# Kernel tuning notes

Measured on AMD Instinct MI355X. Metric: run time of the kernel, lower is better.

## Reference

```python
import jax, jax.numpy as jnp
import numpy as np

N, E, D, A, FC, B = 50000, 800000, 256, 7, 64, 512
EPS = 1e-5

def _glorot(key, fan_in, fan_out):
    lim = np.sqrt(6.0 / (fan_in + fan_out))
    return jax.random.uniform(key, (fan_in, fan_out), jnp.float32, -lim, lim)

def setup_inputs() -> dict:
    key = jax.random.key(0)
    ks = jax.random.split(key, 20)
    inp = {
        'x': jax.random.normal(ks[0], (N, 3), jnp.float32),
        'edge_index': jax.random.randint(ks[1], (2, E), 0, N, jnp.int32),
        'batch_index': jnp.sort(jax.random.randint(ks[2], (N,), 0, B, jnp.int32)),
        'a': jax.random.normal(ks[3], (B, A), jnp.float32),
        # GCNConv weights (lin weight + bias)
        'W0': _glorot(ks[4], 3, D),   'b0': jnp.zeros((D,), jnp.float32),
        'W1': _glorot(ks[5], D, D),   'b1': jnp.zeros((D,), jnp.float32),
        'W2': _glorot(ks[6], D, D),   'b2': jnp.zeros((D,), jnp.float32),
        'W3': _glorot(ks[7], D, D),   'b3': jnp.zeros((D,), jnp.float32),
        # action MLP
        'afc1_w': _glorot(ks[8], A, 8 * A),     'afc1_b': jnp.zeros((8 * A,), jnp.float32),
        'afc2_w': _glorot(ks[9], 8 * A, 8 * A), 'afc2_b': jnp.zeros((8 * A,), jnp.float32),
        'afc3_w': _glorot(ks[10], 8 * A, D),    'afc3_b': jnp.zeros((D,), jnp.float32),
        # head
        'fc1_w': _glorot(ks[11], D, FC), 'fc1_b': jnp.zeros((FC,), jnp.float32),
        'fc2_w': _glorot(ks[12], FC, 1), 'fc2_b': jnp.zeros((1,), jnp.float32),
        # LayerNorm affine params
        'ln1_g': jnp.ones((D,), jnp.float32),  'ln1_b': jnp.zeros((D,), jnp.float32),
        'ln2_g': jnp.ones((D,), jnp.float32),  'ln2_b': jnp.zeros((D,), jnp.float32),
        'ln4_g': jnp.ones((FC,), jnp.float32), 'ln4_b': jnp.zeros((FC,), jnp.float32),
        'ln5_g': jnp.ones((8 * A,), jnp.float32), 'ln5_b': jnp.zeros((8 * A,), jnp.float32),
    }
    return inp

def leaky(x):
    return jnp.where(x >= 0, x, 0.01 * x)

def layernorm(x, g, b):
    m = jnp.mean(x, axis=-1, keepdims=True)
    v = jnp.mean((x - m) ** 2, axis=-1, keepdims=True)
    return (x - m) * jax.lax.rsqrt(v + EPS) * g + b

def reference(x, edge_index, batch_index, a,
              W0, b0, W1, b1, W2, b2, W3, b3,
              afc1_w, afc1_b, afc2_w, afc2_b, afc3_w, afc3_b,
              fc1_w, fc1_b, fc2_w, fc2_b,
              ln1_g, ln1_b, ln2_g, ln2_b, ln4_g, ln4_b, ln5_g, ln5_b):
    n = x.shape[0]
    loop = jnp.arange(n, dtype=edge_index.dtype)
    src = jnp.concatenate([edge_index[0], loop])  # message sources
    dst = jnp.concatenate([edge_index[1], loop])  # message targets
    # symmetric GCN normalization with self-loops: deg over targets
    deg = jax.ops.segment_sum(jnp.ones_like(dst, dtype=x.dtype), dst, num_segments=n)
    dinv = jnp.where(deg > 0, jax.lax.rsqrt(deg), 0.0)
    norm = (dinv[src] * dinv[dst])[:, None]  # [E+N, 1]

    def gcn(h, W, bias):
        hw = h @ W
        agg = jax.ops.segment_sum(hw[src] * norm, dst, num_segments=n)
        return agg + bias

    h0 = gcn(x, W0, b0)
    h1 = leaky(gcn(h0, W1, b1)) + h0
    h2 = leaky(gcn(h1, W2, b2)) + h1
    h3 = leaky(gcn(h2, W3, b3)) + h2

    pooled = jax.ops.segment_max(h3, batch_index, num_segments=B)  # [B, D]
    V = layernorm(pooled, ln2_g, ln2_b)

    av = leaky(a @ afc1_w + afc1_b)
    av = layernorm(av, ln5_g, ln5_b)
    av = leaky(av @ afc2_w + afc2_b)
    av = leaky(av @ afc3_w + afc3_b)
    av = layernorm(av, ln1_g, ln1_b)

    z = V * av
    z = layernorm(leaky(z @ fc1_w + fc1_b), ln4_g, ln4_b)
    out = z @ fc2_w + fc2_b
    return out[:, 0]
```

## Files before the change

kernel.cpp:

```cpp
#include <hip/hip_runtime.h>

#define LN_EPS 1e-5f
#define SCAN_CHUNK 4096

typedef __bf16 bf16x8 __attribute__((ext_vector_type(8)));
typedef float f32x4 __attribute__((ext_vector_type(4)));
typedef float f32x2 __attribute__((ext_vector_type(2)));

__device__ __forceinline__ float b2f(unsigned short s) {
    union { unsigned u; float f; } c; c.u = ((unsigned)s) << 16; return c.f;
}
__device__ __forceinline__ unsigned short f2b(float f) {
    union { float f; unsigned u; } c; c.f = f;
    unsigned r = (c.u + 0x7FFFu + ((c.u >> 16) & 1u)) >> 16;
    return (unsigned short)r;
}
__device__ __forceinline__ f32x2 up2(unsigned u) {
    union { unsigned u; float f; } lo, hi;
    lo.u = u << 16; hi.u = u & 0xffff0000u;
    f32x2 r; r.x = lo.f; r.y = hi.f; return r;
}
__device__ __forceinline__ unsigned pk2(f32x2 v) {
    return ((unsigned)f2b(v.y) << 16) | (unsigned)f2b(v.x);
}
__device__ __forceinline__ float leaky(float x) { return x >= 0.f ? x : 0.01f * x; }
__device__ __forceinline__ unsigned encf(float f) {
    union { float f; unsigned u; } c; c.f = f;
    return ((int)c.u < 0) ? ~c.u : (c.u | 0x80000000u);
}
__device__ __forceinline__ float decf(unsigned u) {
    union { unsigned u; float f; } c;
    c.u = (u & 0x80000000u) ? (u & 0x7FFFFFFFu) : ~u;
    return c.f;
}


__global__ void init_kernel(int* ec, int* fill, int n) {
    int i = blockIdx.x * 256 + threadIdx.x;
    if (i < n) { ec[i] = 0; fill[i] = 0; }
}

__global__ void deg_kernel(const int* __restrict__ dst, int* ec, int e) {
    int i = blockIdx.x * 256 + threadIdx.x;
    if (i < e) atomicAdd(&ec[dst[i]], 1);
}

__global__ void scanA(const int* __restrict__ ec, int* __restrict__ bsum, int n) {
    __shared__ int red[4];
    int b = blockIdx.x, t = threadIdx.x;
    int base = b * SCAN_CHUNK + t * 16;
    int s = 0;
    #pragma unroll
    for (int k = 0; k < 16; ++k) { int i = base + k; if (i < n) s += (ec[i] + 7) & ~7; }
    #pragma unroll
    for (int off = 32; off; off >>= 1) s += __shfl_down(s, off, 64);
    if ((t & 63) == 0) red[t >> 6] = s;
    __syncthreads();
    if (t == 0) bsum[b] = red[0] + red[1] + red[2] + red[3];
}

__global__ void scanB(int* bsum, int nb) {
    if (threadIdx.x == 0) {
        int acc = 0;
        for (int i = 0; i < nb; ++i) { int v = bsum[i]; bsum[i] = acc; acc += v; }
        bsum[nb] = acc;
    }
}

__global__ void scanC(const int* __restrict__ ec, const int* __restrict__ bsum,
                      int* __restrict__ ptr, int n, int nb) {
    __shared__ int wsum[4];
    int b = blockIdx.x, t = threadIdx.x, lane = t & 63, w = t >> 6;
    int base = b * SCAN_CHUNK + t * 16;
    int loc[16]; int s = 0;
    #pragma unroll
    for (int k = 0; k < 16; ++k) {
        int i = base + k; int v = (i < n) ? ((ec[i] + 7) & ~7) : 0;
        loc[k] = s; s += v;
    }
    int x = s;
    #pragma unroll
    for (int off = 1; off < 64; off <<= 1) { int y = __shfl_up(x, off, 64); if (lane >= off) x += y; }
    if (lane == 63) wsum[w] = x;
    __syncthreads();
    int wexcl = 0;
    #pragma unroll
    for (int ww = 0; ww < 4; ++ww) if (ww < w) wexcl += wsum[ww];
    int toff = bsum[b] + wexcl + (x - s);
    #pragma unroll
    for (int k = 0; k < 16; ++k) { int i = base + k; if (i < n) ptr[i] = toff + loc[k]; }
    if (b == nb - 1 && t == 255) ptr[n] = bsum[nb];
}

__global__ void dinv_kernel(const int* __restrict__ ec, float* __restrict__ dinv, int n, int mpad) {
    int i = blockIdx.x * 256 + threadIdx.x;
    if (i < mpad) dinv[i] = (i < n) ? rsqrtf((float)(ec[i] + 1)) : 0.f;
}

__global__ void xp_kernel(const float* __restrict__ x, const float* __restrict__ dinv,
                          float4* __restrict__ xp, int n, int mpad) {
    int i = blockIdx.x * 256 + threadIdx.x;
    if (i >= mpad) return;
    float4 v = make_float4(0.f, 0.f, 0.f, 0.f);
    if (i < n) {
        float d = dinv[i];
        v.x = d * x[i * 3]; v.y = d * x[i * 3 + 1]; v.z = d * x[i * 3 + 2];
    }
    xp[i] = v;
}

__global__ void csrc_init_kernel(const int* __restrict__ ptr, int* __restrict__ csrc, int n) {
    int i = blockIdx.x * 256 + threadIdx.x;
    if (i < ptr[n]) csrc[i] = n << 6;
}

__global__ void fill_kernel(const int* __restrict__ src, const int* __restrict__ dst,
                            const int* __restrict__ ptr, int* fill,
                            int* __restrict__ csrc, int e) {
    int i = blockIdx.x * 256 + threadIdx.x;
    if (i < e) {
        int d = dst[i];
        int pos = atomicAdd(&fill[d], 1);
        csrc[ptr[d] + pos] = src[i] << 6;
    }
}


__global__ void wt_kernel(const float* __restrict__ W1, const float* __restrict__ W2,
                          const float* __restrict__ W3, unsigned short* __restrict__ wt) {
    int k = blockIdx.x, l = blockIdx.y, nn = threadIdx.x;
    const float* W = (l == 0) ? W1 : (l == 1) ? W2 : W3;
    wt[l * 65536 + nn * 256 + k] = f2b(W[k * 256 + nn]);
}


__global__ void aggx_kernel(const float4* __restrict__ xp, const float* __restrict__ dinv,
                            const int* __restrict__ ptr, const int* __restrict__ csrc,
                            float* __restrict__ aggx, int n) {
    int i = blockIdx.x * 256 + threadIdx.x;
    if (i >= n) return;
    const char* xb = (const char*)xp;
    float4 self = xp[i];
    float a0 = self.x, a1 = self.y, a2 = self.z;
    float p0 = 0.f, p1 = 0.f, p2 = 0.f;
    float q0 = 0.f, q1 = 0.f, q2 = 0.f;
    float r0 = 0.f, r1 = 0.f, r2 = 0.f;
    int e0 = ptr[i], e1 = ptr[i + 1];
    for (int e = e0; e < e1; e += 4) {
        int4 v = *(const int4*)(csrc + e);
        float4 u0 = *(const float4*)(xb + (((unsigned)v.x) >> 2));
        float4 u1 = *(const float4*)(xb + (((unsigned)v.y) >> 2));
        float4 u2 = *(const float4*)(xb + (((unsigned)v.z) >> 2));
        float4 u3 = *(const float4*)(xb + (((unsigned)v.w) >> 2));
        a0 += u0.x; a1 += u0.y; a2 += u0.z;
        p0 += u1.x; p1 += u1.y; p2 += u1.z;
        q0 += u2.x; q1 += u2.y; q2 += u2.z;
        r0 += u3.x; r1 += u3.y; r2 += u3.z;
    }
    a0 += (p0 + q0) + r0; a1 += (p1 + q1) + r1; a2 += (p2 + q2) + r2;
    float di = dinv[i];
    aggx[i * 3] = a0 * di; aggx[i * 3 + 1] = a1 * di; aggx[i * 3 + 2] = a2 * di;
}

__global__ __launch_bounds__(256) void h0_kernel(const float* __restrict__ aggx,
                          const float* __restrict__ W0, const float* __restrict__ b0,
                          const float* __restrict__ dinv,
                          float* __restrict__ h, unsigned short* __restrict__ hbs,
                          int n, int mpad) {
    int t = threadIdx.x;
    int row = blockIdx.x * 4 + (t >> 6);
    int f = (t & 63) * 4;
    if (row >= mpad) return;
    unsigned short* hp = hbs + ((size_t)(f >> 5) * mpad + row) * 32 + (f & 31);
    if (row < n) {
        float a0 = aggx[row * 3], a1 = aggx[row * 3 + 1], a2 = aggx[row * 3 + 2];
        float4 w0 = *(const float4*)(W0 + f);
        float4 w1 = *(const float4*)(W0 + 256 + f);
        float4 w2 = *(const float4*)(W0 + 512 + f);
        float4 bb = *(const float4*)(b0 + f);
        float4 v;
        v.x = bb.x + a0 * w0.x + a1 * w1.x + a2 * w2.x;
        v.y = bb.y + a0 * w0.y + a1 * w1.y + a2 * w2.y;
        v.z = bb.z + a0 * w0.z + a1 * w1.z + a2 * w2.z;
        v.w = bb.w + a0 * w0.w + a1 * w1.w + a2 * w2.w;
        *(float4*)(h + (size_t)row * 256 + f) = v;
        float di = dinv[row];
        ushort4 o;
        o.x = f2b(di * v.x); o.y = f2b(di * v.y); o.z = f2b(di * v.z); o.w = f2b(di * v.w);
        *(ushort4*)hp = o;
    } else {
        ushort4 o; o.x = 0; o.y = 0; o.z = 0; o.w = 0;
        *(ushort4*)hp = o;
    }
}


__global__ __launch_bounds__(256) void spmm_kernel(
    const unsigned short* __restrict__ hbs,
    const int* __restrict__ ptr, const int* __restrict__ csrc,
    const float* __restrict__ dinv,
    unsigned short* __restrict__ agg,
    int n, int mpad) {
    int chunk = blockIdx.x & 7;
    int g = blockIdx.x >> 3;
    int t = threadIdx.x;
    int node = g * 64 + (t >> 2);
    if (node >= n) return;
    unsigned loff = (unsigned)((t & 3) << 4);
    const char* cb = (const char*)hbs + (size_t)chunk * mpad * 64;
    int e0 = ptr[node], e1 = ptr[node + 1];
    uint4 own = *(const uint4*)(cb + (((unsigned)node << 6) | loff));
    f32x2 accA0 = up2(own.x), accA1 = up2(own.y), accA2 = up2(own.z), accA3 = up2(own.w);
    f32x2 accB0 = (f32x2)(0.f), accB1 = (f32x2)(0.f), accB2 = (f32x2)(0.f), accB3 = (f32x2)(0.f);
    int e = e0;
    int4 ia, ib;
    if (e < e1) { ia = *(const int4*)(csrc + e); ib = *(const int4*)(csrc + e + 4); }
    while (e < e1) {
        int en = e + 8;
        int4 na, nb;
        if (en < e1) { na = *(const int4*)(csrc + en); nb = *(const int4*)(csrc + en + 4); }
        uint4 u0 = *(const uint4*)(cb + ((unsigned)ia.x | loff));
        uint4 u1 = *(const uint4*)(cb + ((unsigned)ia.y | loff));
        uint4 u2 = *(const uint4*)(cb + ((unsigned)ia.z | loff));
        uint4 u3 = *(const uint4*)(cb + ((unsigned)ia.w | loff));
        uint4 u4 = *(const uint4*)(cb + ((unsigned)ib.x | loff));
        uint4 u5 = *(const uint4*)(cb + ((unsigned)ib.y | loff));
        uint4 u6 = *(const uint4*)(cb + ((unsigned)ib.z | loff));
        uint4 u7 = *(const uint4*)(cb + ((unsigned)ib.w | loff));
        accA0 += up2(u0.x); accA1 += up2(u0.y); accA2 += up2(u0.z); accA3 += up2(u0.w);
        accB0 += up2(u1.x); accB1 += up2(u1.y); accB2 += up2(u1.z); accB3 += up2(u1.w);
        accA0 += up2(u2.x); accA1 += up2(u2.y); accA2 += up2(u2.z); accA3 += up2(u2.w);
        accB0 += up2(u3.x); accB1 += up2(u3.y); accB2 += up2(u3.z); accB3 += up2(u3.w);
        accA0 += up2(u4.x); accA1 += up2(u4.y); accA2 += up2(u4.z); accA3 += up2(u4.w);
        accB0 += up2(u5.x); accB1 += up2(u5.y); accB2 += up2(u5.z); accB3 += up2(u5.w);
        accA0 += up2(u6.x); accA1 += up2(u6.y); accA2 += up2(u6.z); accA3 += up2(u6.w);
        accB0 += up2(u7.x); accB1 += up2(u7.y); accB2 += up2(u7.z); accB3 += up2(u7.w);
        ia = na; ib = nb; e = en;
    }
    float di = dinv[node];
    f32x2 dd; dd.x = di; dd.y = di;
    accA0 = (accA0 + accB0) * dd;
    accA1 = (accA1 + accB1) * dd;
    accA2 = (accA2 + accB2) * dd;
    accA3 = (accA3 + accB3) * dd;
    uint4 o;
    o.x = pk2(accA0); o.y = pk2(accA1); o.z = pk2(accA2); o.w = pk2(accA3);
    *(uint4*)((char*)agg + (size_t)chunk * mpad * 64 + (((unsigned)node << 6) | loff)) = o;
}


__global__ __launch_bounds__(256) void gemm_kernel(const unsigned short* __restrict__ A,
                                                   const unsigned short* __restrict__ Bt,
                                                   const float* __restrict__ bias,
                                                   const float* __restrict__ dinv,
                                                   float* __restrict__ h,
                                                   unsigned short* __restrict__ hbs,
                                                   const int* __restrict__ batch,
                                                   unsigned* __restrict__ pooledu,
                                                   int mpad, int n, int write_hbs, int last) {
    const int K = 256;
    __shared__ int sb[64];
    int wid = threadIdx.x >> 6, lane = threadIdx.x & 63;
    int m0 = blockIdx.x * 64;
    if (last && threadIdx.x < 64) {
        int r = m0 + threadIdx.x;
        sb[threadIdx.x] = (r < n) ? batch[r] : -1;
    }
    __syncthreads();
    int n0 = wid * 64;
    int lr = lane & 15, lg = lane >> 4;
    f32x4 acc[4][4];
    #pragma unroll
    for (int i = 0; i < 4; i++)
        #pragma unroll
        for (int j = 0; j < 4; j++) acc[i][j] = (f32x4)(0.f);
    const unsigned short* Ap = A + ((size_t)(m0 + lr)) * 32 + lg * 8;
    const unsigned short* Bp = Bt + (size_t)(n0 + lr) * K + lg * 8;
    #pragma unroll
    for (int kc = 0; kc < 8; ++kc) {
        bf16x8 af[4], bfr[4];
        #pragma unroll
        for (int mi = 0; mi < 4; mi++)
            af[mi] = *(const bf16x8*)(Ap + (size_t)kc * mpad * 32 + mi * 512);
        #pragma unroll
        for (int ni = 0; ni < 4; ni++)
            bfr[ni] = *(const bf16x8*)(Bp + (size_t)ni * 16 * K + kc * 32);
        #pragma unroll
        for (int mi = 0; mi < 4; mi++)
            #pragma unroll
            for (int ni = 0; ni < 4; ni++)
                acc[mi][ni] = __builtin_amdgcn_mfma_f32_16x16x32_bf16(af[mi], bfr[ni], acc[mi][ni], 0, 0, 0);
    }
    if (!last) {
        #pragma unroll
        for (int mi = 0; mi < 4; mi++) {
            int r0 = m0 + mi * 16 + lg * 4;
            float4 dv = *(const float4*)(dinv + r0);
            #pragma unroll
            for (int ni = 0; ni < 4; ni++) {
                int c = n0 + ni * 16 + lr;
                float bv = bias[c];
                int ch = c >> 5, cf = c & 31;
                float vr[4];
                #pragma unroll
                for (int j = 0; j < 4; ++j) {
                    size_t ho = (size_t)(r0 + j) * 256 + c;
                    float v = leaky(acc[mi][ni][j] + bv) + h[ho];
                    h[ho] = v;
                    vr[j] = v;
                }
                if (write_hbs) {
                    unsigned short* hp = hbs + ((size_t)ch * mpad + r0) * 32 + cf;
                    hp[0]  = f2b(vr[0] * dv.x);
                    hp[32] = f2b(vr[1] * dv.y);
                    hp[64] = f2b(vr[2] * dv.z);
                    hp[96] = f2b(vr[3] * dv.w);
                }
            }
        }
    } else {
        #pragma unroll
        for (int ni = 0; ni < 4; ni++) {
            int c = n0 + ni * 16 + lr;
            float bv = bias[c];
            int cs = -1; float cm = 0.f;
            #pragma unroll
            for (int mi = 0; mi < 4; mi++) {
                int rb = mi * 16 + lg * 4;
                #pragma unroll
                for (int j = 0; j < 4; ++j) {
                    int seg = sb[rb + j];
                    float v = leaky(acc[mi][ni][j] + bv) + h[(size_t)(m0 + rb + j) * 256 + c];
                    if (seg >= 0) {
                        if (seg != cs) {
                            if (cs >= 0) atomicMax(pooledu + (size_t)cs * 256 + c, encf(cm));
                            cs = seg; cm = v;
                        } else {
                            cm = fmaxf(cm, v);
                        }
                    }
                }
            }
            if (cs >= 0) atomicMax(pooledu + (size_t)cs * 256 + c, encf(cm));
        }
    }
}

__global__ void pool_init_kernel(unsigned* pooledu) {
    pooledu[blockIdx.x * 256 + threadIdx.x] = 0u;
}


__device__ __forceinline__ float blk_sum(float v, float* red) {
    #pragma unroll
    for (int off = 32; off; off >>= 1) v += __shfl_down(v, off, 64);
    int lane = threadIdx.x & 63, wid = threadIdx.x >> 6;
    if (lane == 0) red[wid] = v;
    __syncthreads();
    float s = red[0] + red[1] + red[2] + red[3];
    __syncthreads();
    return s;
}

__global__ __launch_bounds__(256) void head_kernel(
    const unsigned* __restrict__ pooledu, const float* __restrict__ a,
    const float* __restrict__ afc1_w, const float* __restrict__ afc1_b,
    const float* __restrict__ afc2_w, const float* __restrict__ afc2_b,
    const float* __restrict__ afc3_w, const float* __restrict__ afc3_b,
    const float* __restrict__ fc1_w, const float* __restrict__ fc1_b,
    const float* __restrict__ fc2_w, const float* __restrict__ fc2_b,
    const float* __restrict__ ln1_g, const float* __restrict__ ln1_b,
    const float* __restrict__ ln2_g, const float* __restrict__ ln2_b,
    const float* __restrict__ ln4_g, const float* __restrict__ ln4_b,
    const float* __restrict__ ln5_g, const float* __restrict__ ln5_b,
    float* __restrict__ out) {
    __shared__ float red[4];
    __shared__ float sM[2];
    __shared__ float s1[56], s2[56], sZ[256], sT[64];
    int b = blockIdx.x, tid = threadIdx.x;

    float pv = decf(pooledu[(size_t)b * 256 + tid]);
    float m = blk_sum(pv, red) * (1.f / 256.f);
    float d0 = pv - m;
    float var = blk_sum(d0 * d0, red) * (1.f / 256.f);
    float V = d0 * rsqrtf(var + LN_EPS) * ln2_g[tid] + ln2_b[tid];

    if (tid < 56) {
        float acc = afc1_b[tid];
        #pragma unroll
        for (int k = 0; k < 7; ++k) acc += a[b * 7 + k] * afc1_w[k * 56 + tid];
        s1[tid] = leaky(acc);
    }
    __syncthreads();
    if (tid == 0) {
        float s = 0.f; for (int k = 0; k < 56; ++k) s += s1[k];
        float mm = s / 56.f;
        float q = 0.f; for (int k = 0; k < 56; ++k) { float d = s1[k] - mm; q += d * d; }
        sM[0] = mm; sM[1] = rsqrtf(q / 56.f + LN_EPS);
    }
    __syncthreads();
    if (tid < 56) s1[tid] = (s1[tid] - sM[0]) * sM[1] * ln5_g[tid] + ln5_b[tid];
    __syncthreads();
    if (tid < 56) {
        float acc = afc2_b[tid];
        for (int k = 0; k < 56; ++k) acc += s1[k] * afc2_w[k * 56 + tid];
        s2[tid] = leaky(acc);
    }
    __syncthreads();
    float acc = afc3_b[tid];
    for (int k = 0; k < 56; ++k) acc += s2[k] * afc3_w[k * 256 + tid];
    acc = leaky(acc);
    m = blk_sum(acc, red) * (1.f / 256.f);
    d0 = acc - m;
    var = blk_sum(d0 * d0, red) * (1.f / 256.f);
    float av = d0 * rsqrtf(var + LN_EPS) * ln1_g[tid] + ln1_b[tid];

    float z = V * av;
    sZ[tid] = z;
    __syncthreads();
    if (tid < 64) {
        float a2 = fc1_b[tid];
        for (int k = 0; k < 256; ++k) a2 += sZ[k] * fc1_w[k * 64 + tid];
        sT[tid] = leaky(a2);
    }
    __syncthreads();
    if (tid == 0) {
        float s = 0.f; for (int k = 0; k < 64; ++k) s += sT[k];
        float mm = s / 64.f;
        float q = 0.f; for (int k = 0; k < 64; ++k) { float d = sT[k] - mm; q += d * d; }
        float r = rsqrtf(q / 64.f + LN_EPS);
        float o = fc2_b[0];
        for (int k = 0; k < 64; ++k) {
            float zz = (sT[k] - mm) * r * ln4_g[k] + ln4_b[k];
            o += zz * fc2_w[k];
        }
        out[b] = o;
    }
}


extern "C" void kernel_launch(void* const* d_in, const int* in_sizes, int n_in,
                              void* d_out, int out_size, void* d_ws, size_t ws_size,
                              hipStream_t stream) {
    const float* x     = (const float*)d_in[0];
    const int*   eidx  = (const int*)d_in[1];
    const int*   batch = (const int*)d_in[2];
    const float* a     = (const float*)d_in[3];
    const float* W0 = (const float*)d_in[4];  const float* b0 = (const float*)d_in[5];
    const float* W1 = (const float*)d_in[6];  const float* b1 = (const float*)d_in[7];
    const float* W2 = (const float*)d_in[8];  const float* b2 = (const float*)d_in[9];
    const float* W3 = (const float*)d_in[10]; const float* b3 = (const float*)d_in[11];
    const float* afc1_w = (const float*)d_in[12]; const float* afc1_b = (const float*)d_in[13];
    const float* afc2_w = (const float*)d_in[14]; const float* afc2_b = (const float*)d_in[15];
    const float* afc3_w = (const float*)d_in[16]; const float* afc3_b = (const float*)d_in[17];
    const float* fc1_w  = (const float*)d_in[18]; const float* fc1_b  = (const float*)d_in[19];
    const float* fc2_w  = (const float*)d_in[20]; const float* fc2_b  = (const float*)d_in[21];
    const float* ln1_g = (const float*)d_in[22]; const float* ln1_b = (const float*)d_in[23];
    const float* ln2_g = (const float*)d_in[24]; const float* ln2_b = (const float*)d_in[25];
    const float* ln4_g = (const float*)d_in[26]; const float* ln4_b = (const float*)d_in[27];
    const float* ln5_g = (const float*)d_in[28]; const float* ln5_b = (const float*)d_in[29];

    int N = in_sizes[0] / 3;
    int E = in_sizes[1] / 2;
    int B = in_sizes[3] / 7;
    int Mpad = ((N + 63) / 64) * 64;
    int NB = (N + SCAN_CHUNK - 1) / SCAN_CHUNK;
    int Ecap = E + 7 * N + 8;

    char* p = (char*)d_ws;
    auto alloc = [&](size_t bytes) -> char* {
        char* r = p; p += (bytes + 255) & ~(size_t)255; return r;
    };
    int*   ec   = (int*)alloc((size_t)N * 4);
    int*   fill = (int*)alloc((size_t)N * 4);
    int*   ptr  = (int*)alloc((size_t)(N + 1) * 4);
    int*   bsum = (int*)alloc((size_t)(NB + 1) * 4);
    int*   csrc = (int*)alloc((size_t)Ecap * 4);
    float* dinv = (float*)alloc((size_t)Mpad * 4);
    float4* xp  = (float4*)alloc((size_t)Mpad * 16);
    float* aggx = (float*)alloc((size_t)N * 3 * 4);
    float* h    = (float*)alloc((size_t)Mpad * 256 * 4);
    unsigned short* hbs = (unsigned short*)alloc((size_t)Mpad * 256 * 2);
    unsigned short* agg = (unsigned short*)alloc((size_t)Mpad * 256 * 2);
    unsigned short* wt  = (unsigned short*)alloc((size_t)3 * 65536 * 2);
    unsigned* pooledu = (unsigned*)alloc((size_t)B * 256 * 4);

    const int* srcl = eidx;
    const int* dstl = eidx + E;

    init_kernel<<<(N + 255) / 256, 256, 0, stream>>>(ec, fill, N);
    deg_kernel<<<(E + 255) / 256, 256, 0, stream>>>(dstl, ec, E);
    scanA<<<NB, 256, 0, stream>>>(ec, bsum, N);
    scanB<<<1, 64, 0, stream>>>(bsum, NB);
    scanC<<<NB, 256, 0, stream>>>(ec, bsum, ptr, N, NB);
    dinv_kernel<<<(Mpad + 255) / 256, 256, 0, stream>>>(ec, dinv, N, Mpad);
    xp_kernel<<<(Mpad + 255) / 256, 256, 0, stream>>>(x, dinv, xp, N, Mpad);
    csrc_init_kernel<<<(Ecap + 255) / 256, 256, 0, stream>>>(ptr, csrc, N);
    fill_kernel<<<(E + 255) / 256, 256, 0, stream>>>(srcl, dstl, ptr, fill, csrc, E);
    wt_kernel<<<dim3(256, 3), 256, 0, stream>>>(W1, W2, W3, wt);
    aggx_kernel<<<(N + 255) / 256, 256, 0, stream>>>(xp, dinv, ptr, csrc, aggx, N);
    h0_kernel<<<Mpad / 4, 256, 0, stream>>>(aggx, W0, b0, dinv, h, hbs, N, Mpad);
    pool_init_kernel<<<B, 256, 0, stream>>>(pooledu);

    const float* biases[3] = { b1, b2, b3 };
    int nblkN = (N + 63) / 64;
    for (int l = 0; l < 3; ++l) {
        spmm_kernel<<<nblkN * 8, 256, 0, stream>>>(hbs, ptr, csrc, dinv, agg, N, Mpad);
        gemm_kernel<<<Mpad / 64, 256, 0, stream>>>(agg, wt + (size_t)l * 65536, biases[l],
                                                   dinv, h, hbs, batch, pooledu,
                                                   Mpad, N, (l < 2) ? 1 : 0, (l == 2) ? 1 : 0);
    }

    head_kernel<<<B, 256, 0, stream>>>(pooledu, a,
        afc1_w, afc1_b, afc2_w, afc2_b, afc3_w, afc3_b,
        fc1_w, fc1_b, fc2_w, fc2_b,
        ln1_g, ln1_b, ln2_g, ln2_b, ln4_g, ln4_b, ln5_g, ln5_b,
        (float*)d_out);
}
```

Measured before the change: 561.3 us.

## Drop fp32 residual buffer; rebuild residual from scaled bf16 features and merge setup kernels

Removes the fp32 hidden-state array h (Mpad×256 floats) that was read and written in every GEMM epilogue. The residual is now recovered from the bf16 dinv-scaled copy hbs by multiplying by sqrt(degree), using a new sdeg array. The epilogue updates hbs in place. It also merges dinv, xp and csrc padding initialisation into one node_setup kernel, which pads only the per-node tail slots. In exchange, the residual path now runs in bf16, adding rounding error that accumulates across layers.

After: 506.1 us. -9.8%, faster.

```diff
diff --git a/kernel.cpp b/kernel.cpp
--- a/kernel.cpp
+++ b/kernel.cpp
@@ -92,26 +92,25 @@
     if (b == nb - 1 && t == 255) ptr[n] = bsum[nb];
 }
 
-__global__ void dinv_kernel(const int* __restrict__ ec, float* __restrict__ dinv, int n, int mpad) {
-    int i = blockIdx.x * 256 + threadIdx.x;
-    if (i < mpad) dinv[i] = (i < n) ? rsqrtf((float)(ec[i] + 1)) : 0.f;
-}
-
-__global__ void xp_kernel(const float* __restrict__ x, const float* __restrict__ dinv,
-                          float4* __restrict__ xp, int n, int mpad) {
+__global__ void node_setup(const float* __restrict__ x, const int* __restrict__ ec,
+                           const int* __restrict__ ptr,
+                           float* __restrict__ dinv, float* __restrict__ sdeg,
+                           float4* __restrict__ xp, int* __restrict__ csrc,
+                           int n, int mpad) {
     int i = blockIdx.x * 256 + threadIdx.x;
     if (i >= mpad) return;
+    float dv = 0.f, sv = 0.f;
     float4 v = make_float4(0.f, 0.f, 0.f, 0.f);
     if (i < n) {
-        float d = dinv[i];
-        v.x = d * x[i * 3]; v.y = d * x[i * 3 + 1]; v.z = d * x[i * 3 + 2];
-    }
-    xp[i] = v;
-}
-
-__global__ void csrc_init_kernel(const int* __restrict__ ptr, int* __restrict__ csrc, int n) {
-    int i = blockIdx.x * 256 + threadIdx.x;
-    if (i < ptr[n]) csrc[i] = n << 6;
+        int e = ec[i];
+        float dg = (float)(e + 1);
+        dv = rsqrtf(dg); sv = sqrtf(dg);
+        v.x = dv * x[i * 3]; v.y = dv * x[i * 3 + 1]; v.z = dv * x[i * 3 + 2];
+        int p0 = ptr[i] + e, p1 = ptr[i] + ((e + 7) & ~7);
+        int pad = n << 6;
+        for (int j = p0; j < p1; ++j) csrc[j] = pad;
+    }
+    dinv[i] = dv; sdeg[i] = sv; xp[i] = v;
 }
 
 __global__ void fill_kernel(const int* __restrict__ src, const int* __restrict__ dst,
@@ -165,7 +164,7 @@
 __global__ __launch_bounds__(256) void h0_kernel(const float* __restrict__ aggx,
                           const float* __restrict__ W0, const float* __restrict__ b0,
                           const float* __restrict__ dinv,
-                          float* __restrict__ h, unsigned short* __restrict__ hbs,
+                          unsigned short* __restrict__ hbs,
                           int n, int mpad) {
     int t = threadIdx.x;
     int row = blockIdx.x * 4 + (t >> 6);
@@ -183,7 +182,6 @@
         v.y = bb.y + a0 * w0.y + a1 * w1.y + a2 * w2.y;
         v.z = bb.z + a0 * w0.z + a1 * w1.z + a2 * w2.z;
         v.w = bb.w + a0 * w0.w + a1 * w1.w + a2 * w2.w;
-        *(float4*)(h + (size_t)row * 256 + f) = v;
         float di = dinv[row];
         ushort4 o;
         o.x = f2b(di * v.x); o.y = f2b(di * v.y); o.z = f2b(di * v.z); o.w = f2b(di * v.w);
@@ -253,11 +251,11 @@
                                                    const unsigned short* __restrict__ Bt,
                                                    const float* __restrict__ bias,
                                                    const float* __restrict__ dinv,
-                                                   float* __restrict__ h,
+                                                   const float* __restrict__ sdeg,
                                                    unsigned short* __restrict__ hbs,
                                                    const int* __restrict__ batch,
                                                    unsigned* __restrict__ pooledu,
-                                                   int mpad, int n, int write_hbs, int last) {
+                                                   int mpad, int n, int last) {
     const int K = 256;
     __shared__ int sb[64];
     int wid = threadIdx.x >> 6, lane = threadIdx.x & 63;
@@ -296,26 +294,25 @@
         for (int mi = 0; mi < 4; mi++) {
             int r0 = m0 + mi * 16 + lg * 4;
             float4 dv = *(const float4*)(dinv + r0);
+            float4 sv = *(const float4*)(sdeg + r0);
             #pragma unroll
             for (int ni = 0; ni < 4; ni++) {
                 int c = n0 + ni * 16 + lr;
                 float bv = bias[c];
                 int ch = c >> 5, cf = c & 31;
-                float vr[4];
-                #pragma unroll
-                for (int j = 0; j < 4; ++j) {
-                    size_t ho = (size_t)(r0 + j) * 256 + c;
-                    float v = leaky(acc[mi][ni][j] + bv) + h[ho];
-                    h[ho] = v;
-                    vr[j] = v;
-                }
-                if (write_hbs) {
-                    unsigned short* hp = hbs + ((size_t)ch * mpad + r0) * 32 + cf;
-                    hp[0]  = f2b(vr[0] * dv.x);
-                    hp[32] = f2b(vr[1] * dv.y);
-                    hp[64] = f2b(vr[2] * dv.z);
-                    hp[96] = f2b(vr[3] * dv.w);
-                }
+                unsigned short* hp = hbs + ((size_t)ch * mpad + r0) * 32 + cf;
+                float h0o = b2f(hp[0])  * sv.x;
+                float h1o = b2f(hp[32]) * sv.y;
+                float h2o = b2f(hp[64]) * sv.z;
+                float h3o = b2f(hp[96]) * sv.w;
+                float v0 = leaky(acc[mi][ni][0] + bv) + h0o;
+                float v1 = leaky(acc[mi][ni][1] + bv) + h1o;
+                float v2 = leaky(acc[mi][ni][2] + bv) + h2o;
+                float v3 = leaky(acc[mi][ni][3] + bv) + h3o;
+                hp[0]  = f2b(v0 * dv.x);
+                hp[32] = f2b(v1 * dv.y);
+                hp[64] = f2b(v2 * dv.z);
+                hp[96] = f2b(v3 * dv.w);
             }
         }
     } else {
@@ -323,14 +320,18 @@
         for (int ni = 0; ni < 4; ni++) {
             int c = n0 + ni * 16 + lr;
             float bv = bias[c];
+            int ch = c >> 5, cf = c & 31;
+            const unsigned short* hpb = hbs + (size_t)ch * mpad * 32 + cf;
             int cs = -1; float cm = 0.f;
             #pragma unroll
             for (int mi = 0; mi < 4; mi++) {
                 int rb = mi * 16 + lg * 4;
                 #pragma unroll
                 for (int j = 0; j < 4; ++j) {
+                    int row = m0 + rb + j;
                     int seg = sb[rb + j];
-                    float v = leaky(acc[mi][ni][j] + bv) + h[(size_t)(m0 + rb + j) * 256 + c];
+                    float ho = b2f(hpb[(size_t)row * 32]) * sdeg[row];
+                    float v = leaky(acc[mi][ni][j] + bv) + ho;
                     if (seg >= 0) {
                         if (seg != cs) {
                             if (cs >= 0) atomicMax(pooledu + (size_t)cs * 256 + c, encf(cm));
@@ -477,9 +478,9 @@
     int*   bsum = (int*)alloc((size_t)(NB + 1) * 4);
     int*   csrc = (int*)alloc((size_t)Ecap * 4);
     float* dinv = (float*)alloc((size_t)Mpad * 4);
+    float* sdeg = (float*)alloc((size_t)Mpad * 4);
     float4* xp  = (float4*)alloc((size_t)Mpad * 16);
     float* aggx = (float*)alloc((size_t)N * 3 * 4);
-    float* h    = (float*)alloc((size_t)Mpad * 256 * 4);
     unsigned short* hbs = (unsigned short*)alloc((size_t)Mpad * 256 * 2);
     unsigned short* agg = (unsigned short*)alloc((size_t)Mpad * 256 * 2);
     unsigned short* wt  = (unsigned short*)alloc((size_t)3 * 65536 * 2);
@@ -493,13 +494,11 @@
     scanA<<<NB, 256, 0, stream>>>(ec, bsum, N);
     scanB<<<1, 64, 0, stream>>>(bsum, NB);
     scanC<<<NB, 256, 0, stream>>>(ec, bsum, ptr, N, NB);
-    dinv_kernel<<<(Mpad + 255) / 256, 256, 0, stream>>>(ec, dinv, N, Mpad);
-    xp_kernel<<<(Mpad + 255) / 256, 256, 0, stream>>>(x, dinv, xp, N, Mpad);
-    csrc_init_kernel<<<(Ecap + 255) / 256, 256, 0, stream>>>(ptr, csrc, N);
+    node_setup<<<(Mpad + 255) / 256, 256, 0, stream>>>(x, ec, ptr, dinv, sdeg, xp, csrc, N, Mpad);
     fill_kernel<<<(E + 255) / 256, 256, 0, stream>>>(srcl, dstl, ptr, fill, csrc, E);
     wt_kernel<<<dim3(256, 3), 256, 0, stream>>>(W1, W2, W3, wt);
     aggx_kernel<<<(N + 255) / 256, 256, 0, stream>>>(xp, dinv, ptr, csrc, aggx, N);
-    h0_kernel<<<Mpad / 4, 256, 0, stream>>>(aggx, W0, b0, dinv, h, hbs, N, Mpad);
+    h0_kernel<<<Mpad / 4, 256, 0, stream>>>(aggx, W0, b0, dinv, hbs, N, Mpad);
     pool_init_kernel<<<B, 256, 0, stream>>>(pooledu);
 
     const float* biases[3] = { b1, b2, b3 };
@@ -507,8 +506,8 @@
     for (int l = 0; l < 3; ++l) {
         spmm_kernel<<<nblkN * 8, 256, 0, stream>>>(hbs, ptr, csrc, dinv, agg, N, Mpad);
         gemm_kernel<<<Mpad / 64, 256, 0, stream>>>(agg, wt + (size_t)l * 65536, biases[l],
-                                                   dinv, h, hbs, batch, pooledu,
-                                                   Mpad, N, (l < 2) ? 1 : 0, (l == 2) ? 1 : 0);
+                                                   dinv, sdeg, hbs, batch, pooledu,
+                                                   Mpad, N, (l == 2) ? 1 : 0);
     }
 
     head_kernel<<<B, 256, 0, stream>>>(pooledu, a,
```
